# Optimization experiments

Measured on AMD Instinct MI355X. Metric: run time of the kernel, lower is better.

Reference implementation:

```python
import jax, jax.numpy as jnp
import numpy as np

N = 50000   # nodes
E = 800000  # edges
G = 256     # graphs in batch
NF, EF, H, L = 16, 8, 128, 4
EPS = 1e-5


def setup_inputs() -> dict:
    key = jax.random.key(0)
    ks = jax.random.split(key, 20)
    s = 0.05
    return {
        "x": jax.random.normal(ks[0], (N, NF), jnp.float32),
        "edge_index": jax.random.randint(ks[1], (2, E), 0, N, dtype=jnp.int32),
        "edge_attr": jax.random.uniform(ks[2], (E, EF), jnp.float32),
        "batch": jnp.sort(jax.random.randint(ks[3], (N,), 0, G, dtype=jnp.int32)),
        "W_emb": jax.random.normal(ks[4], (NF, H), jnp.float32) * s,
        "b_emb": jnp.zeros((H,), jnp.float32),
        "Wf": jax.random.normal(ks[5], (L, 2 * H + EF, H), jnp.float32) * s,
        "bf": jnp.zeros((L, H), jnp.float32),
        "Ws": jax.random.normal(ks[6], (L, 2 * H + EF, H), jnp.float32) * s,
        "bs": jnp.zeros((L, H), jnp.float32),
        "gamma": jnp.ones((L, H), jnp.float32),
        "beta": jnp.zeros((L, H), jnp.float32),
        "W1": jax.random.normal(ks[7], (H, 64), jnp.float32) * s,
        "b1": jnp.zeros((64,), jnp.float32),
        "W2": jax.random.normal(ks[8], (64, 32), jnp.float32) * s,
        "b2": jnp.zeros((32,), jnp.float32),
        "W_out": jax.random.normal(ks[9], (32, 1), jnp.float32) * s,
        "b_out": jnp.zeros((1,), jnp.float32),
    }


def reference(x, edge_index, edge_attr, batch, W_emb, b_emb, Wf, bf, Ws, bs,
              gamma, beta, W1, b1, W2, b2, W_out, b_out):
    src, dst = edge_index[0], edge_index[1]  # message j->i: x_j=h[src], x_i=h[dst]
    h = jax.nn.relu(x @ W_emb + b_emb)       # [N, H]
    for l in range(L):
        # CGConv: z_ij = [x_i, x_j, e_ij]; gated message; sum-aggregate; +x residual
        z = jnp.concatenate([h[dst], h[src], edge_attr], axis=-1)  # [E, 2H+EF]
        m = jax.nn.sigmoid(z @ Wf[l] + bf[l]) * jax.nn.softplus(z @ Ws[l] + bs[l])
        agg = jax.ops.segment_sum(m, dst, num_segments=N)
        x_new = agg + h
        # BatchNorm1d (training-mode batch statistics, biased var)
        mu = x_new.mean(axis=0)
        var = x_new.var(axis=0)
        x_new = gamma[l] * (x_new - mu) * jax.lax.rsqrt(var + EPS) + beta[l]
        x_new = jax.nn.relu(x_new)
        h = h + x_new
    # global mean pool over graphs
    cnt = jax.ops.segment_sum(jnp.ones((N,), h.dtype), batch, num_segments=G)
    pooled = jax.ops.segment_sum(h, batch, num_segments=G) / jnp.maximum(cnt, 1.0)[:, None]
    g = jax.nn.relu(pooled @ W1 + b1)
    g = jax.nn.relu(g @ W2 + b2)
    return (g @ W_out + b_out).squeeze(-1)  # [G]
```

## Files before the change

### kernel.cpp

```cpp
#include <hip/hip_runtime.h>
#include <hip/hip_bf16.h>

#define H 128
#define EFD 8
#define NLAYER 4
#define ZDIM (2*H+EFD)

typedef float f32x2 __attribute__((ext_vector_type(2)));
typedef float f32x4 __attribute__((ext_vector_type(4)));
typedef short s16x8 __attribute__((ext_vector_type(8)));
typedef _Float16 f16x4 __attribute__((ext_vector_type(4)));

#define PKFMA_LO(acc, a, b) asm("v_pk_fma_f32 %0, %1, %2, %0 op_sel:[0,0,0] op_sel_hi:[0,1,1]" : "+v"(acc) : "v"(a), "v"(b))
#define PKFMA_HI(acc, a, b) asm("v_pk_fma_f32 %0, %1, %2, %0 op_sel:[1,0,0] op_sel_hi:[1,1,1]" : "+v"(acc) : "v"(a), "v"(b))
#define PKFMA_LO_INIT(dst, a, b, c) asm("v_pk_fma_f32 %0, %1, %2, %3 op_sel:[0,0,0] op_sel_hi:[0,1,1]" : "=v"(dst) : "v"(a), "v"(b), "v"(c))

#define L2E 1.44269504088896340736f
#define LN2 0.69314718055994530942f

__device__ __forceinline__ unsigned short f2bf(float x){
    unsigned u = __float_as_uint(x);
    return (unsigned short)((u + 0x7FFFu + ((u>>16)&1u)) >> 16);
}

__global__ void embed_kernel(const float* __restrict__ x, const float* __restrict__ We,
                             const float* __restrict__ be, float* __restrict__ h, int N){
    int idx = blockIdx.x*blockDim.x + threadIdx.x;
    if (idx >= N*H) return;
    int n = idx >> 7, f = idx & 127;
    float a = be[f];
    #pragma unroll
    for (int k=0;k<16;k++) a = fmaf(x[n*16+k], We[k*H+f], a);
    h[idx] = fmaxf(a, 0.f);
}

__global__ void hist_kernel(const int* __restrict__ dstI, int* __restrict__ counts, int E){
    int e = blockIdx.x*blockDim.x + threadIdx.x;
    if (e < E) atomicAdd(&counts[dstI[e]], 1);
}

__global__ __launch_bounds__(1024) void scan1(const int* __restrict__ counts, int* __restrict__ incl,
                                              int* __restrict__ bsums, int N){
    __shared__ int lds[1024];
    int t = threadIdx.x;
    int i = blockIdx.x*1024 + t;
    int v = (i < N) ? counts[i] : 0;
    lds[t] = v;
    __syncthreads();
    for (int off=1; off<1024; off<<=1){
        int add = (t>=off) ? lds[t-off] : 0;
        __syncthreads();
        lds[t] += add;
        __syncthreads();
    }
    if (i < N) incl[i] = lds[t];
    if (t == 1023) bsums[blockIdx.x] = lds[1023];
}

__global__ void scan2(int* bsums, int nb){
    if (threadIdx.x == 0){
        int run = 0;
        for (int b=0;b<nb;b++){ int v = bsums[b]; bsums[b] = run; run += v; }
    }
}

__global__ __launch_bounds__(1024) void scan3(const int* incl, const int* __restrict__ counts,
                                              const int* __restrict__ bsums, int* __restrict__ rowptr,
                                              int* cursor, int N, int E){
    int i = blockIdx.x*1024 + threadIdx.x;
    if (i >= N) return;
    int ex = incl[i] - counts[i] + bsums[blockIdx.x];
    rowptr[i] = ex;
    cursor[i] = ex;
    if (i == N-1) rowptr[N] = E;
}

__global__ void scatter_kernel(const int* __restrict__ srcI, const int* __restrict__ dstI,
                               const float* __restrict__ eattr, int* __restrict__ cursor,
                               int* __restrict__ src_s, float* __restrict__ ea_s, int E){
    int e = blockIdx.x*blockDim.x + threadIdx.x;
    if (e >= E) return;
    int d = dstI[e];
    int pos = atomicAdd(&cursor[d], 1);
    src_s[pos] = srcI[e];
    const float4* s4 = (const float4*)(eattr + (size_t)e*EFD);
    float4* o4 = (float4*)(ea_s + (size_t)pos*EFD);
    o4[0] = s4[0]; o4[1] = s4[1];
}

__global__ __launch_bounds__(256) void wpack_kernel(const float* __restrict__ Wf, const float* __restrict__ Ws,
        s16x8* __restrict__ bhi, s16x8* __restrict__ blo){
    int idx = blockIdx.x*256 + threadIdx.x;
    int l = idx & 63, ct = (idx>>6)&7, ks = (idx>>9)&3, w = (idx>>11)&3, layer = idx>>13;
    int cp = w*128 + ct*16 + (l&15);
    int k0 = ks*32 + ((l>>4)<<3);
    const float* WfL = Wf + (size_t)layer*ZDIM*H;
    const float* WsL = Ws + (size_t)layer*ZDIM*H;
    int colIn = cp & 127;
    int sel = cp >> 7;
    const float* Wm = (sel & 1) ? WsL : WfL;
    int krow = (sel >> 1) ? H : 0;
    s16x8 vh, vl;
    #pragma unroll
    for (int e=0;e<8;e++){
        float v = Wm[(size_t)(krow + k0 + e)*H + colIn];
        unsigned short hb = f2bf(v);
        float rem = v - __uint_as_float(((unsigned)hb)<<16);
        vh[e] = (short)hb;
        vl[e] = (short)f2bf(rem);
    }
    bhi[idx] = vh;
    blo[idx] = vl;
}

__global__ __launch_bounds__(256, 2) void table_mfma(
        const float* __restrict__ h, const s16x8* __restrict__ bhi, const s16x8* __restrict__ blo,
        const float* __restrict__ bf_l, const float* __restrict__ bs_l,
        float* __restrict__ TD, _Float16* __restrict__ TS16, int N, int layer){
    __shared__ __align__(16) short amat[2][32*136];
    const int t = threadIdx.x;
    const int n0 = blockIdx.x*32;
    {
        const int row = t >> 3, kb = (t & 7)*16;
        const int gn = n0 + row;
        const float* src = h + (size_t)gn*H + kb;
        float vv[16];
        #pragma unroll
        for (int q=0;q<16;q+=4){
            float4 x4 = (gn < N) ? *(const float4*)(src + q) : make_float4(0.f,0.f,0.f,0.f);
            vv[q]=x4.x; vv[q+1]=x4.y; vv[q+2]=x4.z; vv[q+3]=x4.w;
        }
        s16x8 hv[2], lv[2];
        #pragma unroll
        for (int q=0;q<16;q++){
            unsigned short hb = f2bf(vv[q]);
            float rem = vv[q] - __uint_as_float(((unsigned)hb)<<16);
            hv[q>>3][q&7] = (short)hb;
            lv[q>>3][q&7] = (short)f2bf(rem);
        }
        short* dh = &amat[0][row*136 + kb];
        short* dl = &amat[1][row*136 + kb];
        *(s16x8*)dh = hv[0]; *(s16x8*)(dh+8) = hv[1];
        *(s16x8*)dl = lv[0]; *(s16x8*)(dl+8) = lv[1];
    }
    __syncthreads();
    const int lane = t & 63, w = t >> 6;
    const int rbase = lane & 15, kg = lane >> 4;
    f32x4 acc[2][8];
    #pragma unroll
    for (int rt=0;rt<2;rt++)
        #pragma unroll
        for (int ct=0;ct<8;ct++){ acc[rt][ct][0]=0.f; acc[rt][ct][1]=0.f; acc[rt][ct][2]=0.f; acc[rt][ct][3]=0.f; }
    const size_t bbase = ((size_t)layer*4 + w)*2048;
    #pragma unroll
    for (int ks=0;ks<4;ks++){
        s16x8 bh[8], bl[8];
        #pragma unroll
        for (int ct=0;ct<8;ct++){
            bh[ct] = bhi[bbase + ks*512 + ct*64 + lane];
            bl[ct] = blo[bbase + ks*512 + ct*64 + lane];
        }
        s16x8 ah[2], al[2];
        #pragma unroll
        for (int rt=0;rt<2;rt++){
            const int ao = (rbase + 16*rt)*136 + ks*32 + kg*8;
            ah[rt] = *(const s16x8*)&amat[0][ao];
            al[rt] = *(const s16x8*)&amat[1][ao];
        }
        #pragma unroll
        for (int ct=0;ct<8;ct++)
            #pragma unroll
            for (int rt=0;rt<2;rt++){
                acc[rt][ct] = __builtin_amdgcn_mfma_f32_16x16x32_bf16(ah[rt], bh[ct], acc[rt][ct], 0, 0, 0);
                acc[rt][ct] = __builtin_amdgcn_mfma_f32_16x16x32_bf16(ah[rt], bl[ct], acc[rt][ct], 0, 0, 0);
                acc[rt][ct] = __builtin_amdgcn_mfma_f32_16x16x32_bf16(al[rt], bh[ct], acc[rt][ct], 0, 0, 0);
            }
    }
    if (w < 2){
        float* outb = TD;
        const int colbase = (w & 1)*128;
        const float* bias = (w == 0) ? bf_l : bs_l;
        #pragma unroll
        for (int ct=0;ct<8;ct++){
            const int c_local = ct*16 + rbase;
            const float bv = bias[c_local]*L2E;
            #pragma unroll
            for (int rt=0;rt<2;rt++){
                const int nrow0 = n0 + 16*rt + kg*4;
                #pragma unroll
                for (int r=0;r<4;r++){
                    const int nd = nrow0 + r;
                    if (nd < N) outb[(size_t)nd*256 + colbase + c_local] = fmaf(acc[rt][ct][r], L2E, bv);
                }
            }
        }
    } else {
        const int slot = (w & 1) << 1;
        #pragma unroll
        for (int ct=0;ct<8;ct++){
            const int c_local = ct*16 + rbase;
            const int off = (c_local >> 1)*4 + slot + (c_local & 1);
            #pragma unroll
            for (int rt=0;rt<2;rt++){
                const int nrow0 = n0 + 16*rt + kg*4;
                #pragma unroll
                for (int r=0;r<4;r++){
                    const int nd = nrow0 + r;
                    if (nd < N) TS16[(size_t)nd*256 + off] = (_Float16)(acc[rt][ct][r]*L2E);
                }
            }
        }
    }
}

__global__ __launch_bounds__(256, 4) void agg_kernel(
        const float* __restrict__ TD, const _Float16* __restrict__ TS16,
        const int* __restrict__ rowptr, const int* __restrict__ src_s, const float* __restrict__ ea_s,
        const float* __restrict__ Wf_l, const float* __restrict__ Ws_l,
        const float* __restrict__ h, float* __restrict__ xn, int N){
    __shared__ float wE[2048];
    const int t = threadIdx.x;
    {
        const float4* a = (const float4*)(Wf_l + 2*H*H);
        const float4* b = (const float4*)(Ws_l + 2*H*H);
        float4 va = a[t], vb = b[t];
        va.x*=L2E; va.y*=L2E; va.z*=L2E; va.w*=L2E;
        vb.x*=L2E; vb.y*=L2E; vb.z*=L2E; vb.w*=L2E;
        ((float4*)wE)[t] = va;
        ((float4*)wE)[256 + t] = vb;
    }
    __syncthreads();
    const int k = t & 63;
    const int i = blockIdx.x*4 + (t >> 6);
    if (i >= N) return;
    f32x2 wef2[8], wes2[8];
    #pragma unroll
    for (int r=0;r<8;r++){
        wef2[r] = *(const f32x2*)&wE[r*128 + 2*k];
        wes2[r] = *(const f32x2*)&wE[1024 + r*128 + 2*k];
    }
    #pragma unroll
    for (int r=0;r<8;r++) asm volatile("" : "+v"(wef2[r]), "+v"(wes2[r]));
    const f32x2* td = (const f32x2*)(TD + ((size_t)i << 8));
    f32x2 fd2 = td[k], sd2 = td[64+k];
    f32x2 acc = {0.f, 0.f};
    const int e0 = __builtin_amdgcn_readfirstlane(rowptr[i]);
    const int e1 = __builtin_amdgcn_readfirstlane(rowptr[i+1]);
    int j = (e0 < e1) ? __builtin_amdgcn_readfirstlane(src_s[e0]) : 0;
    for (int e = e0; e < e1; ++e){
        const _Float16* tsrow = TS16 + ((size_t)(unsigned)j << 8);
        f16x4 tv = *(const f16x4*)(tsrow + 4*k);
        const int en = (e+1 < e1) ? (e+1) : e;
        const int jn = __builtin_amdgcn_readfirstlane(src_s[en]);
        const float* eb = ea_s + (size_t)e*EFD;
        f32x4 eaA = *(const f32x4*)(eb);
        f32x4 eaB = *(const f32x4*)(eb+4);
        f32x2 ea0 = __builtin_shufflevector(eaA, eaA, 0, 1);
        f32x2 ea1 = __builtin_shufflevector(eaA, eaA, 2, 3);
        f32x2 ea2 = __builtin_shufflevector(eaB, eaB, 0, 1);
        f32x2 ea3 = __builtin_shufflevector(eaB, eaB, 2, 3);
        f32x2 ef, es;
        PKFMA_LO_INIT(ef, ea0, wef2[0], fd2);
        PKFMA_HI(ef, ea0, wef2[1]);
        PKFMA_LO(ef, ea1, wef2[2]); PKFMA_HI(ef, ea1, wef2[3]);
        PKFMA_LO(ef, ea2, wef2[4]); PKFMA_HI(ef, ea2, wef2[5]);
        PKFMA_LO(ef, ea3, wef2[6]); PKFMA_HI(ef, ea3, wef2[7]);
        PKFMA_LO_INIT(es, ea0, wes2[0], sd2);
        PKFMA_HI(es, ea0, wes2[1]);
        PKFMA_LO(es, ea1, wes2[2]); PKFMA_HI(es, ea1, wes2[3]);
        PKFMA_LO(es, ea2, wes2[4]); PKFMA_HI(es, ea2, wes2[5]);
        PKFMA_LO(es, ea3, wes2[6]); PKFMA_HI(es, ea3, wes2[7]);
        f32x2 fs2 = {(float)tv[0], (float)tv[1]};
        f32x2 ss2 = {(float)tv[2], (float)tv[3]};
        f32x2 g = ef + fs2;
        f32x2 p = es + ss2;
        float sx = __builtin_amdgcn_rcpf(1.0f + __builtin_amdgcn_exp2f(-g.x));
        float sy = __builtin_amdgcn_rcpf(1.0f + __builtin_amdgcn_exp2f(-g.y));
        float tx = fmaxf(p.x, 0.f) + __builtin_amdgcn_logf(1.0f + __builtin_amdgcn_exp2f(-fabsf(p.x)));
        float ty = fmaxf(p.y, 0.f) + __builtin_amdgcn_logf(1.0f + __builtin_amdgcn_exp2f(-fabsf(p.y)));
        acc.x = fmaf(sx*tx, LN2, acc.x);
        acc.y = fmaf(sy*ty, LN2, acc.y);
        j = jn;
    }
    f32x2 hv = *(const f32x2*)(h + ((size_t)i << 7) + 2*k);
    f32x2 o = acc + hv;
    *(f32x2*)(xn + ((size_t)i << 7) + 2*k) = o;
}

__global__ __launch_bounds__(256) void stats_kernel(const float* __restrict__ xn, double* __restrict__ sums, int N){
    __shared__ double l1[128], l2[128];
    const int f = threadIdx.x & 127;
    const int half = threadIdx.x >> 7;
    const int nb = gridDim.x;
    const int per = (N + nb - 1)/nb;
    const int r0 = blockIdx.x*per;
    const int r1 = min(N, r0+per);
    double s = 0.0, s2 = 0.0;
    for (int r=r0+half; r<r1; r+=2){
        float v = xn[(size_t)r*H + f];
        s += v; s2 += (double)v*(double)v;
    }
    if (half == 1){ l1[f] = s; l2[f] = s2; }
    __syncthreads();
    if (half == 0){
        s += l1[f]; s2 += l2[f];
        atomicAdd(&sums[f], s);
        atomicAdd(&sums[H+f], s2);
    }
}

__global__ void finalize_bn(double* __restrict__ sums, const float* __restrict__ gamma_l,
                            const float* __restrict__ beta_l, float* __restrict__ scsh, int N){
    int f = threadIdx.x;
    if (f >= H) return;
    double mu = sums[f]/(double)N;
    double var = sums[H+f]/(double)N - mu*mu;
    if (var < 0.0) var = 0.0;
    float sc = (float)((double)gamma_l[f] / sqrt(var + 1e-5));
    scsh[f]   = sc;
    scsh[H+f] = (float)((double)beta_l[f] - mu*(double)sc);
    sums[f] = 0.0;
    sums[H+f] = 0.0;
}

__global__ __launch_bounds__(256) void apply_bn(const float* __restrict__ xn, const float* __restrict__ scsh,
                                                float* __restrict__ h, int total4){
    int idx = blockIdx.x*blockDim.x + threadIdx.x;
    if (idx >= total4) return;
    int f = (idx*4) & (H-1);
    float4 v  = *(const float4*)(xn + (size_t)idx*4);
    float4 hh = *(const float4*)(h  + (size_t)idx*4);
    float4 sc = *(const float4*)(scsh + f);
    float4 sh = *(const float4*)(scsh + H + f);
    hh.x += fmaxf(fmaf(v.x, sc.x, sh.x), 0.f);
    hh.y += fmaxf(fmaf(v.y, sc.y, sh.y), 0.f);
    hh.z += fmaxf(fmaf(v.z, sc.z, sh.z), 0.f);
    hh.w += fmaxf(fmaf(v.w, sc.w, sh.w), 0.f);
    *(float4*)(h + (size_t)idx*4) = hh;
}

__global__ __launch_bounds__(128) void pool_mlp_kernel(const float* __restrict__ h, const int* __restrict__ batch,
        const float* __restrict__ W1, const float* __restrict__ b1,
        const float* __restrict__ W2, const float* __restrict__ b2,
        const float* __restrict__ Wo, const float* __restrict__ bo,
        float* __restrict__ out, int N){
    __shared__ float row[128];
    __shared__ float g1[64];
    __shared__ float g2[32];
    const int g = blockIdx.x;
    const int t = threadIdx.x;
    int lo = 0, hi = N;
    while (lo < hi){ int m = (lo+hi)>>1; if (batch[m] < g) lo = m+1; else hi = m; }
    const int s0 = lo;
    hi = N;
    while (lo < hi){ int m = (lo+hi)>>1; if (batch[m] < g+1) lo = m+1; else hi = m; }
    const int s1 = lo;
    float acc = 0.f;
    for (int r = s0; r < s1; ++r) acc += h[(size_t)r*H + t];
    const float inv = 1.0f/fmaxf((float)(s1-s0), 1.0f);
    row[t] = acc*inv;
    __syncthreads();
    if (t < 64){
        float a = b1[t];
        #pragma unroll 4
        for (int i2=0;i2<128;i2++) a = fmaf(row[i2], W1[i2*64+t], a);
        g1[t] = fmaxf(a, 0.f);
    }
    __syncthreads();
    if (t < 32){
        float b = b2[t];
        #pragma unroll 4
        for (int i2=0;i2<64;i2++) b = fmaf(g1[i2], W2[i2*32+t], b);
        g2[t] = fmaxf(b, 0.f);
    }
    __syncthreads();
    if (t < 64){
        float p = (t < 32) ? g2[t]*Wo[t] : 0.f;
        for (int off=32; off>0; off>>=1) p += __shfl_down(p, off);
        if (t == 0) out[g] = p + bo[0];
    }
}

extern "C" void kernel_launch(void* const* d_in, const int* in_sizes, int n_in,
                              void* d_out, int out_size, void* d_ws, size_t ws_size,
                              hipStream_t stream){
    const float* x     = (const float*)d_in[0];
    const int*   eidx  = (const int*)d_in[1];
    const float* eattr = (const float*)d_in[2];
    const int*   batch = (const int*)d_in[3];
    const float* W_emb = (const float*)d_in[4];
    const float* b_emb = (const float*)d_in[5];
    const float* Wf    = (const float*)d_in[6];
    const float* bf    = (const float*)d_in[7];
    const float* Wsm   = (const float*)d_in[8];
    const float* bs    = (const float*)d_in[9];
    const float* gamma = (const float*)d_in[10];
    const float* beta  = (const float*)d_in[11];
    const float* W1    = (const float*)d_in[12];
    const float* b1    = (const float*)d_in[13];
    const float* W2    = (const float*)d_in[14];
    const float* b2    = (const float*)d_in[15];
    const float* Wo    = (const float*)d_in[16];
    const float* bo    = (const float*)d_in[17];
    float* out = (float*)d_out;

    const int N = in_sizes[0]/16;
    const int E = in_sizes[1]/2;
    const int G = out_size;

    const int* srcI = eidx;
    const int* dstI = eidx + E;

    char* p = (char*)d_ws;
    auto alloc = [&](size_t bytes)->char*{ char* r = p; p += (bytes + 255) & ~255ull; return r; };
    float*     h      = (float*)     alloc((size_t)N*H*4);
    float*     xn     = (float*)     alloc((size_t)N*H*4);
    float*     TD     = (float*)     alloc((size_t)N*2*H*4);
    _Float16*  TS16   = (_Float16*)  alloc((size_t)N*2*H*2);
    float*     ea_s   = (float*)     alloc((size_t)E*EFD*4);
    int*       src_s  = (int*)       alloc((size_t)E*4);
    int*       rowptr = (int*)       alloc((size_t)(N+1)*4);
    int*       cursor = (int*)       alloc((size_t)N*4);
    int*       counts = (int*)       alloc((size_t)N*4);
    int*       bsums  = (int*)       alloc(256*4);
    double*    sums   = (double*)    alloc(2*H*8);
    float*     scsh   = (float*)     alloc(2*H*4);
    s16x8*     bhi    = (s16x8*)     alloc((size_t)NLAYER*8192*16);
    s16x8*     blo    = (s16x8*)     alloc((size_t)NLAYER*8192*16);

    const int thr = 256;
    hipMemsetAsync(counts, 0, (size_t)N*4, stream);
    hipMemsetAsync(sums, 0, 2*H*8, stream);
    embed_kernel<<<(N*H + thr-1)/thr, thr, 0, stream>>>(x, W_emb, b_emb, h, N);
    hist_kernel<<<(E + thr-1)/thr, thr, 0, stream>>>(dstI, counts, E);
    int nb = (N + 1023)/1024;
    scan1<<<nb, 1024, 0, stream>>>(counts, cursor, bsums, N);
    scan2<<<1, 64, 0, stream>>>(bsums, nb);
    scan3<<<nb, 1024, 0, stream>>>(cursor, counts, bsums, rowptr, cursor, N, E);
    scatter_kernel<<<(E + thr-1)/thr, thr, 0, stream>>>(srcI, dstI, eattr, cursor, src_s, ea_s, E);
    wpack_kernel<<<128, 256, 0, stream>>>(Wf, Wsm, bhi, blo);

    for (int l=0;l<NLAYER;l++){
        const float* Wf_l = Wf  + (size_t)l*ZDIM*H;
        const float* Ws_l = Wsm + (size_t)l*ZDIM*H;
        table_mfma<<<(N+31)/32, 256, 0, stream>>>(h, bhi, blo, bf + l*H, bs + l*H, TD, TS16, N, l);
        agg_kernel<<<(N+3)/4, 256, 0, stream>>>(TD, TS16, rowptr, src_s, ea_s, Wf_l, Ws_l, h, xn, N);
        stats_kernel<<<256, 256, 0, stream>>>(xn, sums, N);
        finalize_bn<<<1, 128, 0, stream>>>(sums, gamma + l*H, beta + l*H, scsh, N);
        apply_bn<<<((N*H/4) + thr-1)/thr, thr, 0, stream>>>(xn, scsh, h, N*H/4);
    }

    pool_mlp_kernel<<<G, 128, 0, stream>>>(h, batch, W1, b1, W2, b2, Wo, bo, out, N);
}
```

Baseline: 935.5 us.

## Fuse BatchNorm apply into next layer's table kernel and pooling; batch edge index loads

Removes the separate apply_bn kernel. The BN scale/shift, ReLU and residual update now run in the prologue of the next layer's table_mfma, which writes h back, and in the final pooling kernel. The aggregation loop is also restructured so that each wave loads up to 64 source indices with one coalesced load and reads them through readlane, with the next TS16 row prefetched one edge ahead. This saves one full read-modify-write pass over h per layer and shortens the serial index-load chain, at the cost of a heavier table prologue.

```diff
diff --git a/kernel.cpp b/kernel.cpp
--- a/kernel.cpp
+++ b/kernel.cpp
@@ -114,7 +114,8 @@
 }
 
 __global__ __launch_bounds__(256, 2) void table_mfma(
-        const float* __restrict__ h, const s16x8* __restrict__ bhi, const s16x8* __restrict__ blo,
+        float* __restrict__ h, const float* __restrict__ xn, const float* __restrict__ scsh,
+        const s16x8* __restrict__ bhi, const s16x8* __restrict__ blo,
         const float* __restrict__ bf_l, const float* __restrict__ bs_l,
         float* __restrict__ TD, _Float16* __restrict__ TS16, int N, int layer){
     __shared__ __align__(16) short amat[2][32*136];
@@ -123,25 +124,52 @@
     {
         const int row = t >> 3, kb = (t & 7)*16;
         const int gn = n0 + row;
-        const float* src = h + (size_t)gn*H + kb;
+        const bool valid = gn < N;
+        float* hr = h + (size_t)gn*H + kb;
         float vv[16];
-        #pragma unroll
-        for (int q=0;q<16;q+=4){
-            float4 x4 = (gn < N) ? *(const float4*)(src + q) : make_float4(0.f,0.f,0.f,0.f);
-            vv[q]=x4.x; vv[q+1]=x4.y; vv[q+2]=x4.z; vv[q+3]=x4.w;
-        }
-        s16x8 hv[2], lv[2];
+        if (scsh){
+            float sc[16], sh[16];
+            #pragma unroll
+            for (int q=0;q<16;q+=4){
+                *(float4*)&sc[q] = *(const float4*)(scsh + kb + q);
+                *(float4*)&sh[q] = *(const float4*)(scsh + H + kb + q);
+            }
+            const float* xr = xn + (size_t)gn*H + kb;
+            #pragma unroll
+            for (int q=0;q<16;q+=4){
+                float4 xv = valid ? *(const float4*)(xr + q) : make_float4(0.f,0.f,0.f,0.f);
+                float4 hv = valid ? *(const float4*)(hr + q) : make_float4(0.f,0.f,0.f,0.f);
+                vv[q]   = hv.x + fmaxf(fmaf(xv.x, sc[q],   sh[q]),   0.f);
+                vv[q+1] = hv.y + fmaxf(fmaf(xv.y, sc[q+1], sh[q+1]), 0.f);
+                vv[q+2] = hv.z + fmaxf(fmaf(xv.z, sc[q+2], sh[q+2]), 0.f);
+                vv[q+3] = hv.w + fmaxf(fmaf(xv.w, sc[q+3], sh[q+3]), 0.f);
+            }
+            if (valid){
+                #pragma unroll
+                for (int q=0;q<16;q+=4){
+                    float4 o; o.x=vv[q]; o.y=vv[q+1]; o.z=vv[q+2]; o.w=vv[q+3];
+                    *(float4*)(hr + q) = o;
+                }
+            }
+        } else {
+            #pragma unroll
+            for (int q=0;q<16;q+=4){
+                float4 hv = valid ? *(const float4*)(hr + q) : make_float4(0.f,0.f,0.f,0.f);
+                vv[q]=hv.x; vv[q+1]=hv.y; vv[q+2]=hv.z; vv[q+3]=hv.w;
+            }
+        }
+        s16x8 hv2[2], lv2[2];
         #pragma unroll
         for (int q=0;q<16;q++){
             unsigned short hb = f2bf(vv[q]);
             float rem = vv[q] - __uint_as_float(((unsigned)hb)<<16);
-            hv[q>>3][q&7] = (short)hb;
-            lv[q>>3][q&7] = (short)f2bf(rem);
+            hv2[q>>3][q&7] = (short)hb;
+            lv2[q>>3][q&7] = (short)f2bf(rem);
         }
         short* dh = &amat[0][row*136 + kb];
         short* dl = &amat[1][row*136 + kb];
-        *(s16x8*)dh = hv[0]; *(s16x8*)(dh+8) = hv[1];
-        *(s16x8*)dl = lv[0]; *(s16x8*)(dl+8) = lv[1];
+        *(s16x8*)dh = hv2[0]; *(s16x8*)(dh+8) = hv2[1];
+        *(s16x8*)dl = lv2[0]; *(s16x8*)(dl+8) = lv2[1];
     }
     __syncthreads();
     const int lane = t & 63, w = t >> 6;
@@ -246,41 +274,44 @@
     f32x2 acc = {0.f, 0.f};
     const int e0 = __builtin_amdgcn_readfirstlane(rowptr[i]);
     const int e1 = __builtin_amdgcn_readfirstlane(rowptr[i+1]);
-    int j = (e0 < e1) ? __builtin_amdgcn_readfirstlane(src_s[e0]) : 0;
-    for (int e = e0; e < e1; ++e){
-        const _Float16* tsrow = TS16 + ((size_t)(unsigned)j << 8);
-        f16x4 tv = *(const f16x4*)(tsrow + 4*k);
-        const int en = (e+1 < e1) ? (e+1) : e;
-        const int jn = __builtin_amdgcn_readfirstlane(src_s[en]);
-        const float* eb = ea_s + (size_t)e*EFD;
-        f32x4 eaA = *(const f32x4*)(eb);
-        f32x4 eaB = *(const f32x4*)(eb+4);
-        f32x2 ea0 = __builtin_shufflevector(eaA, eaA, 0, 1);
-        f32x2 ea1 = __builtin_shufflevector(eaA, eaA, 2, 3);
-        f32x2 ea2 = __builtin_shufflevector(eaB, eaB, 0, 1);
-        f32x2 ea3 = __builtin_shufflevector(eaB, eaB, 2, 3);
-        f32x2 ef, es;
-        PKFMA_LO_INIT(ef, ea0, wef2[0], fd2);
-        PKFMA_HI(ef, ea0, wef2[1]);
-        PKFMA_LO(ef, ea1, wef2[2]); PKFMA_HI(ef, ea1, wef2[3]);
-        PKFMA_LO(ef, ea2, wef2[4]); PKFMA_HI(ef, ea2, wef2[5]);
-        PKFMA_LO(ef, ea3, wef2[6]); PKFMA_HI(ef, ea3, wef2[7]);
-        PKFMA_LO_INIT(es, ea0, wes2[0], sd2);
-        PKFMA_HI(es, ea0, wes2[1]);
-        PKFMA_LO(es, ea1, wes2[2]); PKFMA_HI(es, ea1, wes2[3]);
-        PKFMA_LO(es, ea2, wes2[4]); PKFMA_HI(es, ea2, wes2[5]);
-        PKFMA_LO(es, ea3, wes2[6]); PKFMA_HI(es, ea3, wes2[7]);
-        f32x2 fs2 = {(float)tv[0], (float)tv[1]};
-        f32x2 ss2 = {(float)tv[2], (float)tv[3]};
-        f32x2 g = ef + fs2;
-        f32x2 p = es + ss2;
-        float sx = __builtin_amdgcn_rcpf(1.0f + __builtin_amdgcn_exp2f(-g.x));
-        float sy = __builtin_amdgcn_rcpf(1.0f + __builtin_amdgcn_exp2f(-g.y));
-        float tx = fmaxf(p.x, 0.f) + __builtin_amdgcn_logf(1.0f + __builtin_amdgcn_exp2f(-fabsf(p.x)));
-        float ty = fmaxf(p.y, 0.f) + __builtin_amdgcn_logf(1.0f + __builtin_amdgcn_exp2f(-fabsf(p.y)));
-        acc.x = fmaf(sx*tx, LN2, acc.x);
-        acc.y = fmaf(sy*ty, LN2, acc.y);
-        j = jn;
+    const int myoff = 4*k;
+    for (int ebase = e0; ebase < e1; ebase += 64){
+        const int ecnt = min(64, e1 - ebase);
+        const int ids = (k < ecnt) ? src_s[ebase + k] : 0;
+        int j = __builtin_amdgcn_readlane(ids, 0);
+        f16x4 tv = *(const f16x4*)(TS16 + (((size_t)(unsigned)j) << 8) + myoff);
+        for (int q = 0; q < ecnt; ++q){
+            const int jn = __builtin_amdgcn_readlane(ids, (q+1 < ecnt) ? (q+1) : q);
+            f16x4 tvn = *(const f16x4*)(TS16 + (((size_t)(unsigned)jn) << 8) + myoff);
+            const float* ep = ea_s + (size_t)(ebase + q)*EFD;
+            f32x4 eaA = *(const f32x4*)(ep);
+            f32x4 eaB = *(const f32x4*)(ep + 4);
+            f32x2 ea0 = __builtin_shufflevector(eaA, eaA, 0, 1);
+            f32x2 ea1 = __builtin_shufflevector(eaA, eaA, 2, 3);
+            f32x2 ea2 = __builtin_shufflevector(eaB, eaB, 0, 1);
+            f32x2 ea3 = __builtin_shufflevector(eaB, eaB, 2, 3);
+            f32x2 ef, es;
+            PKFMA_LO_INIT(ef, ea0, wef2[0], fd2);
+            PKFMA_HI(ef, ea0, wef2[1]);
+            PKFMA_LO(ef, ea1, wef2[2]); PKFMA_HI(ef, ea1, wef2[3]);
+            PKFMA_LO(ef, ea2, wef2[4]); PKFMA_HI(ef, ea2, wef2[5]);
+            PKFMA_LO(ef, ea3, wef2[6]); PKFMA_HI(ef, ea3, wef2[7]);
+            PKFMA_LO_INIT(es, ea0, wes2[0], sd2);
+            PKFMA_HI(es, ea0, wes2[1]);
+            PKFMA_LO(es, ea1, wes2[2]); PKFMA_HI(es, ea1, wes2[3]);
+            PKFMA_LO(es, ea2, wes2[4]); PKFMA_HI(es, ea2, wes2[5]);
+            PKFMA_LO(es, ea3, wes2[6]); PKFMA_HI(es, ea3, wes2[7]);
+            f32x2 g = ef, p = es;
+            g.x += (float)tv[0]; g.y += (float)tv[1];
+            p.x += (float)tv[2]; p.y += (float)tv[3];
+            float sx = __builtin_amdgcn_rcpf(1.0f + __builtin_amdgcn_exp2f(-g.x));
+            float sy = __builtin_amdgcn_rcpf(1.0f + __builtin_amdgcn_exp2f(-g.y));
+            float tx = fmaxf(p.x, 0.f) + __builtin_amdgcn_logf(1.0f + __builtin_amdgcn_exp2f(-fabsf(p.x)));
+            float ty = fmaxf(p.y, 0.f) + __builtin_amdgcn_logf(1.0f + __builtin_amdgcn_exp2f(-fabsf(p.y)));
+            acc.x = fmaf(sx*tx, LN2, acc.x);
+            acc.y = fmaf(sy*ty, LN2, acc.y);
+            tv = tvn;
+        }
     }
     f32x2 hv = *(const f32x2*)(h + ((size_t)i << 7) + 2*k);
     f32x2 o = acc + hv;
@@ -323,23 +354,8 @@
     sums[H+f] = 0.0;
 }
 
-__global__ __launch_bounds__(256) void apply_bn(const float* __restrict__ xn, const float* __restrict__ scsh,
-                                                float* __restrict__ h, int total4){
-    int idx = blockIdx.x*blockDim.x + threadIdx.x;
-    if (idx >= total4) return;
-    int f = (idx*4) & (H-1);
-    float4 v  = *(const float4*)(xn + (size_t)idx*4);
-    float4 hh = *(const float4*)(h  + (size_t)idx*4);
-    float4 sc = *(const float4*)(scsh + f);
-    float4 sh = *(const float4*)(scsh + H + f);
-    hh.x += fmaxf(fmaf(v.x, sc.x, sh.x), 0.f);
-    hh.y += fmaxf(fmaf(v.y, sc.y, sh.y), 0.f);
-    hh.z += fmaxf(fmaf(v.z, sc.z, sh.z), 0.f);
-    hh.w += fmaxf(fmaf(v.w, sc.w, sh.w), 0.f);
-    *(float4*)(h + (size_t)idx*4) = hh;
-}
-
-__global__ __launch_bounds__(128) void pool_mlp_kernel(const float* __restrict__ h, const int* __restrict__ batch,
+__global__ __launch_bounds__(128) void pool_mlp_kernel(const float* __restrict__ h, const float* __restrict__ xn,
+        const float* __restrict__ scsh, const int* __restrict__ batch,
         const float* __restrict__ W1, const float* __restrict__ b1,
         const float* __restrict__ W2, const float* __restrict__ b2,
         const float* __restrict__ Wo, const float* __restrict__ bo,
@@ -355,8 +371,13 @@
     hi = N;
     while (lo < hi){ int m = (lo+hi)>>1; if (batch[m] < g+1) lo = m+1; else hi = m; }
     const int s1 = lo;
+    const float sc = scsh[t], sh = scsh[H+t];
     float acc = 0.f;
-    for (int r = s0; r < s1; ++r) acc += h[(size_t)r*H + t];
+    for (int r = s0; r < s1; ++r){
+        float hv = h[(size_t)r*H + t];
+        float xv = xn[(size_t)r*H + t];
+        acc += hv + fmaxf(fmaf(xv, sc, sh), 0.f);
+    }
     const float inv = 1.0f/fmaxf((float)(s1-s0), 1.0f);
     row[t] = acc*inv;
     __syncthreads();
@@ -443,12 +464,12 @@
     for (int l=0;l<NLAYER;l++){
         const float* Wf_l = Wf  + (size_t)l*ZDIM*H;
         const float* Ws_l = Wsm + (size_t)l*ZDIM*H;
-        table_mfma<<<(N+31)/32, 256, 0, stream>>>(h, bhi, blo, bf + l*H, bs + l*H, TD, TS16, N, l);
+        table_mfma<<<(N+31)/32, 256, 0, stream>>>(h, xn, (l==0)?nullptr:scsh, bhi, blo,
+                                                  bf + l*H, bs + l*H, TD, TS16, N, l);
         agg_kernel<<<(N+3)/4, 256, 0, stream>>>(TD, TS16, rowptr, src_s, ea_s, Wf_l, Ws_l, h, xn, N);
         stats_kernel<<<256, 256, 0, stream>>>(xn, sums, N);
         finalize_bn<<<1, 128, 0, stream>>>(sums, gamma + l*H, beta + l*H, scsh, N);
-        apply_bn<<<((N*H/4) + thr-1)/thr, thr, 0, stream>>>(xn, scsh, h, N*H/4);
-    }
-
-    pool_mlp_kernel<<<G, 128, 0, stream>>>(h, batch, W1, b1, W2, b2, Wo, bo, out, N);
-}
+    }
+
+    pool_mlp_kernel<<<G, 128, 0, stream>>>(h, xn, scsh, batch, W1, b1, W2, b2, Wo, bo, out, N);
+}
```

Measured after the change: 939.1 us. No clear change (+0.4%).
